# Kernel optimization log

Measured on AMD Instinct MI355X. Metric: run time of the kernel, lower is better.

## Reference

```python
import jax, jax.numpy as jnp
import numpy as np
import math

B, S, D, H, L = 4, 2048, 512, 8, 2
HD = D // H
NG = (3, 4, 5)
V = 30000          # n_gram_vocab_size
BASE = 31          # rolling hash base
NPATCH = 16
PLEN = S // NPATCH


def _ln(x, w, b, eps):
    m = x.mean(-1, keepdims=True)
    v = ((x - m) ** 2).mean(-1, keepdims=True)
    return (x - m) * jax.lax.rsqrt(v + eps) * w + b


def setup_inputs() -> dict:
    key = jax.random.key(0)
    ks = jax.random.split(key, 16)

    def nrm(i, shape, std=0.02):
        return jax.random.normal(ks[i], shape, dtype=jnp.float32) * std

    return {
        "byte_seq": jax.random.randint(ks[0], (B, S), 0, 256, dtype=jnp.int32),
        "patch_boundaries": jnp.arange(NPATCH + 1, dtype=jnp.int32) * PLEN,
        "byte_emb": nrm(1, (256, D), 1.0 / math.sqrt(D)),
        "ng_emb": nrm(2, (len(NG), V, D)),
        "tl_qkv_w": nrm(3, (L, 3 * D, D)),
        "tl_qkv_b": jnp.zeros((L, 3 * D), jnp.float32),
        "tl_out_w": nrm(4, (L, D, D)),
        "tl_out_b": jnp.zeros((L, D), jnp.float32),
        "tl_ln1_w": jnp.ones((L, D), jnp.float32),
        "tl_ln1_b": jnp.zeros((L, D), jnp.float32),
        "tl_ln2_w": jnp.ones((L, D), jnp.float32),
        "tl_ln2_b": jnp.zeros((L, D), jnp.float32),
        "tl_ff1_w": nrm(5, (L, 4 * D, D)),
        "tl_ff1_b": jnp.zeros((L, 4 * D), jnp.float32),
        "tl_ff2_w": nrm(6, (L, D, 4 * D)),
        "tl_ff2_b": jnp.zeros((L, D), jnp.float32),
        "ca_qkv_w": nrm(7, (3 * D, D)),
        "ca_qkv_b": jnp.zeros((3 * D,), jnp.float32),
        "ca_out_w": nrm(8, (D, D)),
        "ca_out_b": jnp.zeros((D,), jnp.float32),
        "ca_ln_w": jnp.ones((D,), jnp.float32),
        "ca_ln_b": jnp.zeros((D,), jnp.float32),
        "norm_w": jnp.ones((D,), jnp.float32),
        "norm_b": jnp.zeros((D,), jnp.float32),
    }


def _forward(byte_seq, patch_boundaries, byte_emb, ng_emb,
             tl_qkv_w, tl_qkv_b, tl_out_w, tl_out_b,
             tl_ln1_w, tl_ln1_b, tl_ln2_w, tl_ln2_b,
             tl_ff1_w, tl_ff1_b, tl_ff2_w, tl_ff2_b,
             ca_qkv_w, ca_qkv_b, ca_out_w, ca_out_b, ca_ln_w, ca_ln_b,
             norm_w, norm_b):
    x = byte_emb[byte_seq]                                  # [B,S,D]

    # n-gram rolling hash == polynomial hash mod V; computed in parallel
    # as windowed dot products with modular base powers (exact same values
    # as the sequential rolling-update loop in the torch code).
    ng_scale = 1.0 / (len(NG) + 1)
    for idx, n in enumerate(NG):
        powers = jnp.array([pow(BASE, n - 1 - i, V) for i in range(n)],
                           dtype=byte_seq.dtype)
        windows = jnp.stack([byte_seq[:, j:S - n + 1 + j] for j in range(n)],
                            axis=-1)                        # [B,S-n+1,n]
        h = (windows * powers).sum(-1) % V                   # [B,S-n+1]
        x = x.at[:, n - 1:].add(ng_emb[idx][h] * ng_scale)

    scale = 1.0 / math.sqrt(HD)
    neg = jnp.where(jnp.triu(jnp.ones((S, S), dtype=bool), 1),
                    -jnp.inf, 0.0).astype(x.dtype)           # causal additive mask

    # post-norm TransformerEncoderLayer (relu activation, dropout=0/eval)
    for l in range(L):
        qkv = x @ tl_qkv_w[l].T + tl_qkv_b[l]                # [B,S,3D]
        q, k, v = jnp.split(qkv, 3, axis=-1)
        q = q.reshape(B, S, H, HD).transpose(0, 2, 1, 3)
        k = k.reshape(B, S, H, HD).transpose(0, 2, 1, 3)
        v = v.reshape(B, S, H, HD).transpose(0, 2, 1, 3)
        scores = jnp.einsum('bhqd,bhkd->bhqk', q, k) * scale + neg
        a = jax.nn.softmax(scores, axis=-1)
        o = jnp.einsum('bhqk,bhkd->bhqd', a, v).transpose(0, 2, 1, 3).reshape(B, S, D)
        o = o @ tl_out_w[l].T + tl_out_b[l]
        x = _ln(x + o, tl_ln1_w[l], tl_ln1_b[l], 1e-5)
        ff = jax.nn.relu(x @ tl_ff1_w[l].T + tl_ff1_b[l]) @ tl_ff2_w[l].T + tl_ff2_b[l]
        x = _ln(x + ff, tl_ln2_w[l], tl_ln2_b[l], 1e-5)

    # uniform patch boundaries -> vectorized patch cross-attention
    npatch = patch_boundaries.shape[0] - 1
    plen = S // npatch
    xp = x.reshape(B, npatch, plen, D)
    query = xp.mean(axis=2)                                  # [B,P,D]
    qn = _ln(query, ca_ln_w, ca_ln_b, 1e-6)
    kvn = _ln(xp, ca_ln_w, ca_ln_b, 1e-6)
    wq, wk, wv = jnp.split(ca_qkv_w, 3, axis=0)
    bq, bk, bv = jnp.split(ca_qkv_b, 3)
    q = (qn @ wq.T + bq).reshape(B, npatch, H, HD)
    k = (kvn @ wk.T + bk).reshape(B, npatch, plen, H, HD)
    v = (kvn @ wv.T + bv).reshape(B, npatch, plen, H, HD)
    s = jnp.einsum('bphd,bplhd->bphl', q, k) * scale
    a = jax.nn.softmax(s, axis=-1)
    o = jnp.einsum('bphl,bplhd->bphd', a, v).reshape(B, npatch, D)
    patches = query + (o @ ca_out_w.T + ca_out_b)

    return _ln(x, norm_w, norm_b, 1e-6), _ln(patches, norm_w, norm_b, 1e-6)


def reference(byte_seq, patch_boundaries, byte_emb, ng_emb,
              tl_qkv_w, tl_qkv_b, tl_out_w, tl_out_b,
              tl_ln1_w, tl_ln1_b, tl_ln2_w, tl_ln2_b,
              tl_ff1_w, tl_ff1_b, tl_ff2_w, tl_ff2_b,
              ca_qkv_w, ca_qkv_b, ca_out_w, ca_out_b, ca_ln_w, ca_ln_b,
              norm_w, norm_b):
    return _forward(byte_seq, patch_boundaries, byte_emb, ng_emb,
                    tl_qkv_w, tl_qkv_b, tl_out_w, tl_out_b,
                    tl_ln1_w, tl_ln1_b, tl_ln2_w, tl_ln2_b,
                    tl_ff1_w, tl_ff1_b, tl_ff2_w, tl_ff2_b,
                    ca_qkv_w, ca_qkv_b, ca_out_w, ca_out_b, ca_ln_w, ca_ln_b,
                    norm_w, norm_b)
```

## Files before the change

kernel.cpp:

```cpp
#include <hip/hip_runtime.h>
#include <hip/hip_bf16.h>

#define B_ 4
#define S_ 2048
#define D_ 512
#define H_ 8
#define HD_ 64
#define L_ 2
#define V_ 30000
#define NPATCH_ 16
#define PLEN_ 128

typedef short bf16x8 __attribute__((ext_vector_type(8)));
typedef float f32x4 __attribute__((ext_vector_type(4)));

__device__ __forceinline__ unsigned short f2bf(float f) {
    unsigned u = __float_as_uint(f);
    return (unsigned short)((u + 0x7FFFu + ((u >> 16) & 1u)) >> 16);
}

__global__ __launch_bounds__(256) void cast_kernel(
    const float* __restrict__ src, unsigned short* __restrict__ dst, int n4)
{
    const int i = blockIdx.x * 256 + threadIdx.x;
    if (i >= n4) return;
    const float4 v = *reinterpret_cast<const float4*>(src + (size_t)i * 4);
    ushort4 o;
    o.x = f2bf(v.x); o.y = f2bf(v.y); o.z = f2bf(v.z); o.w = f2bf(v.w);
    *reinterpret_cast<ushort4*>(dst + (size_t)i * 4) = o;
}

__global__ __launch_bounds__(128) void embed_ngram_kernel(
    const int* __restrict__ bytes, const float* __restrict__ byte_emb,
    const float* __restrict__ ng_emb, float* __restrict__ x,
    unsigned short* __restrict__ xb)
{
    const int bs = blockIdx.x;
    const int s  = bs % S_;
    const int b  = bs / S_;
    const int d  = threadIdx.x * 4;
    const int* brow = bytes + (size_t)b * S_;

    const int c = brow[s];
    float4 v = *reinterpret_cast<const float4*>(byte_emb + (size_t)c * D_ + d);

    if (s >= 2) {
        int h = (brow[s-2]*961 + brow[s-1]*31 + brow[s]) % V_;
        const float4 g = *reinterpret_cast<const float4*>(ng_emb + ((size_t)0*V_ + h)*D_ + d);
        v.x += 0.25f*g.x; v.y += 0.25f*g.y; v.z += 0.25f*g.z; v.w += 0.25f*g.w;
    }
    if (s >= 3) {
        int h = (brow[s-3]*29791 + brow[s-2]*961 + brow[s-1]*31 + brow[s]) % V_;
        const float4 g = *reinterpret_cast<const float4*>(ng_emb + ((size_t)1*V_ + h)*D_ + d);
        v.x += 0.25f*g.x; v.y += 0.25f*g.y; v.z += 0.25f*g.z; v.w += 0.25f*g.w;
    }
    if (s >= 4) {
        int h = (brow[s-4]*23521 + brow[s-3]*29791 + brow[s-2]*961 + brow[s-1]*31 + brow[s]) % V_;
        const float4 g = *reinterpret_cast<const float4*>(ng_emb + ((size_t)2*V_ + h)*D_ + d);
        v.x += 0.25f*g.x; v.y += 0.25f*g.y; v.z += 0.25f*g.z; v.w += 0.25f*g.w;
    }
    *reinterpret_cast<float4*>(x + (size_t)bs * D_ + d) = v;
    ushort4 o;
    o.x = f2bf(v.x); o.y = f2bf(v.y); o.z = f2bf(v.z); o.w = f2bf(v.w);
    *reinterpret_cast<ushort4*>(xb + (size_t)bs * D_ + d) = o;
}

template<int DO_RELU, int BF16OUT>
__global__ __launch_bounds__(256) void mgemm_kernel(
    const unsigned short* __restrict__ Xb, const unsigned short* __restrict__ Wb,
    const float* __restrict__ bias, void* __restrict__ Yout,
    int M, int N, int K)
{
    __shared__ unsigned short As[128*64];
    __shared__ unsigned short Bs[128*64];

    const int t    = threadIdx.x;
    const int lane = t & 63;
    const int w    = t >> 6;
    const int bm   = blockIdx.y * 128, bn = blockIdx.x * 128;
    const int l15  = lane & 15, lg = lane >> 4;
    const int wr   = w >> 1, wc = w & 1;

    int srow[4], scol[4];
#pragma unroll
    for (int i = 0; i < 4; ++i) {
        const int off = w*1024 + i*4096 + lane*16;
        srow[i] = off >> 7;
        scol[i] = ((off >> 4) & 7) ^ (srow[i] & 7);
    }

    f32x4 acc[4][4];
#pragma unroll
    for (int mt = 0; mt < 4; ++mt)
#pragma unroll
        for (int nt = 0; nt < 4; ++nt) acc[mt][nt] = (f32x4){0.f,0.f,0.f,0.f};

    for (int kt = 0; kt < K; kt += 64) {
#pragma unroll
        for (int i = 0; i < 4; ++i) {
            const unsigned short* gA = Xb + (size_t)(bm + srow[i]) * K + kt + scol[i]*8;
            const unsigned short* gB = Wb + (size_t)(bn + srow[i]) * K + kt + scol[i]*8;
            __builtin_amdgcn_global_load_lds(
                (const __attribute__((address_space(1))) void*)gA,
                (__attribute__((address_space(3))) void*)&As[w*512 + i*2048], 16, 0, 0);
            __builtin_amdgcn_global_load_lds(
                (const __attribute__((address_space(1))) void*)gB,
                (__attribute__((address_space(3))) void*)&Bs[w*512 + i*2048], 16, 0, 0);
        }
        __syncthreads();

#pragma unroll
        for (int ks = 0; ks < 2; ++ks) {
            const int c16 = (ks*4 + lg) ^ (l15 & 7);
            bf16x8 a[4], b[4];
#pragma unroll
            for (int mt = 0; mt < 4; ++mt)
                a[mt] = *reinterpret_cast<const bf16x8*>(&As[(wr*64 + mt*16 + l15)*64 + c16*8]);
#pragma unroll
            for (int nt = 0; nt < 4; ++nt)
                b[nt] = *reinterpret_cast<const bf16x8*>(&Bs[(wc*64 + nt*16 + l15)*64 + c16*8]);
#pragma unroll
            for (int mt = 0; mt < 4; ++mt)
#pragma unroll
                for (int nt = 0; nt < 4; ++nt)
                    acc[mt][nt] = __builtin_amdgcn_mfma_f32_16x16x32_bf16(
                        a[mt], b[nt], acc[mt][nt], 0, 0, 0);
        }
        __syncthreads();
    }

    float bv[4];
#pragma unroll
    for (int nt = 0; nt < 4; ++nt) bv[nt] = bias[bn + wc*64 + nt*16 + l15];

#pragma unroll
    for (int mt = 0; mt < 4; ++mt) {
#pragma unroll
        for (int nt = 0; nt < 4; ++nt) {
            const int n = bn + wc*64 + nt*16 + l15;
#pragma unroll
            for (int r = 0; r < 4; ++r) {
                const int m = bm + wr*64 + mt*16 + 4*lg + r;
                float v = acc[mt][nt][r] + bv[nt];
                if (DO_RELU) v = fmaxf(v, 0.f);
                if (BF16OUT)
                    ((unsigned short*)Yout)[(size_t)m * N + n] = f2bf(v);
                else
                    ((float*)Yout)[(size_t)m * N + n] = v;
            }
        }
    }
}

__global__ __launch_bounds__(256) void gemm_kernel(
    const float* __restrict__ X, const float* __restrict__ W,
    const float* __restrict__ bias, const float* __restrict__ resid,
    float* __restrict__ Y, int M, int N, int K, int do_relu)
{
    __shared__ float As[16][68];
    __shared__ float Bs[16][68];
    const int tid = threadIdx.x;
    const int bm = blockIdx.y * 64, bn = blockIdx.x * 64;
    const int ty = tid >> 4, tx = tid & 15;
    const int lrow = tid >> 2, lc4 = (tid & 3) * 4;

    float acc[4][4];
#pragma unroll
    for (int i = 0; i < 4; ++i)
#pragma unroll
        for (int j = 0; j < 4; ++j) acc[i][j] = 0.f;

    for (int k0 = 0; k0 < K; k0 += 16) {
        const float4 xv = *reinterpret_cast<const float4*>(X + (size_t)(bm + lrow) * K + k0 + lc4);
        const float4 wv = *reinterpret_cast<const float4*>(W + (size_t)(bn + lrow) * K + k0 + lc4);
        __syncthreads();
        As[lc4+0][lrow] = xv.x; As[lc4+1][lrow] = xv.y;
        As[lc4+2][lrow] = xv.z; As[lc4+3][lrow] = xv.w;
        Bs[lc4+0][lrow] = wv.x; Bs[lc4+1][lrow] = wv.y;
        Bs[lc4+2][lrow] = wv.z; Bs[lc4+3][lrow] = wv.w;
        __syncthreads();
#pragma unroll
        for (int kk = 0; kk < 16; ++kk) {
            float a0 = As[kk][ty*4+0], a1 = As[kk][ty*4+1], a2 = As[kk][ty*4+2], a3 = As[kk][ty*4+3];
            float b0 = Bs[kk][tx*4+0], b1 = Bs[kk][tx*4+1], b2 = Bs[kk][tx*4+2], b3 = Bs[kk][tx*4+3];
            acc[0][0] += a0*b0; acc[0][1] += a0*b1; acc[0][2] += a0*b2; acc[0][3] += a0*b3;
            acc[1][0] += a1*b0; acc[1][1] += a1*b1; acc[1][2] += a1*b2; acc[1][3] += a1*b3;
            acc[2][0] += a2*b0; acc[2][1] += a2*b1; acc[2][2] += a2*b2; acc[2][3] += a2*b3;
            acc[3][0] += a3*b0; acc[3][1] += a3*b1; acc[3][2] += a3*b2; acc[3][3] += a3*b3;
        }
    }

#pragma unroll
    for (int i = 0; i < 4; ++i) {
        const int m = bm + ty*4 + i;
#pragma unroll
        for (int j = 0; j < 4; ++j) {
            const int n = bn + tx*4 + j;
            float v = acc[i][j] + bias[n];
            if (do_relu) v = fmaxf(v, 0.f);
            if (resid) v += resid[(size_t)m * N + n];
            Y[(size_t)m * N + n] = v;
        }
    }
}

__global__ __launch_bounds__(256) void attn_mfma_kernel(
    const unsigned short* __restrict__ qkvb, unsigned short* __restrict__ ob)
{
    __shared__ unsigned short Ks[64*72];
    __shared__ unsigned short Vt[64*72];
    __shared__ unsigned short Plds[4*16*72];

    const int t    = threadIdx.x;
    const int lane = t & 63;
    const int w    = t >> 6;
    const int qp   = blockIdx.x;
    const int bh   = blockIdx.y;
    const int h    = bh & 7;
    const int b    = bh >> 3;

    const unsigned short* base = qkvb + (size_t)b * S_ * 1536;
    const int l15 = lane & 15, lg = lane >> 4;
    const int skey = t >> 2, sd0 = (t & 3) * 16;
    const int sg = sd0 >> 4;
    const int scs = ((skey >> 3) ^ sg) * 8 + (skey & 7);
    unsigned short* pw_base = Plds + w*16*72;

#pragma unroll
    for (int half = 0; half < 2; ++half) {
        const int qb  = half ? (31 - qp) : qp;
        const int q0w = qb * 64 + w * 16;

        bf16x8 qf0, qf1;
        {
            const unsigned short* qr = base + (size_t)(q0w + l15) * 1536 + h*64 + lg*8;
            qf0 = *reinterpret_cast<const bf16x8*>(qr);
            qf1 = *reinterpret_cast<const bf16x8*>(qr + 32);
        }

        f32x4 oacc[4];
#pragma unroll
        for (int i = 0; i < 4; ++i) oacc[i] = (f32x4){0.f,0.f,0.f,0.f};
        float mrow[4] = {-INFINITY,-INFINITY,-INFINITY,-INFINITY};
        float lrow[4] = {0.f,0.f,0.f,0.f};

        const int ntiles = qb + 1;
        for (int tile = 0; tile < ntiles; ++tile) {
            const int kt = tile * 64;
            __syncthreads();
            {
                const unsigned short* srcK = base + (size_t)(kt + skey) * 1536 + 512  + h*64 + sd0;
                const unsigned short* srcV = base + (size_t)(kt + skey) * 1536 + 1024 + h*64 + sd0;
                *reinterpret_cast<bf16x8*>(&Ks[skey*72 + sd0])     = *reinterpret_cast<const bf16x8*>(srcK);
                *reinterpret_cast<bf16x8*>(&Ks[skey*72 + sd0 + 8]) = *reinterpret_cast<const bf16x8*>(srcK + 8);
                bf16x8 v0 = *reinterpret_cast<const bf16x8*>(srcV);
                bf16x8 v1 = *reinterpret_cast<const bf16x8*>(srcV + 8);
#pragma unroll
                for (int j = 0; j < 8; ++j) Vt[(sd0+j)*72 + scs]   = (unsigned short)v0[j];
#pragma unroll
                for (int j = 0; j < 8; ++j) Vt[(sd0+8+j)*72 + scs] = (unsigned short)v1[j];
            }
            __syncthreads();

            f32x4 sacc[4];
#pragma unroll
            for (int kt16 = 0; kt16 < 4; ++kt16) {
                sacc[kt16] = (f32x4){0.f,0.f,0.f,0.f};
                const unsigned short* kp = &Ks[(kt16*16 + l15)*72 + lg*8];
                bf16x8 k0 = *reinterpret_cast<const bf16x8*>(kp);
                bf16x8 k1 = *reinterpret_cast<const bf16x8*>(kp + 32);
                sacc[kt16] = __builtin_amdgcn_mfma_f32_16x16x32_bf16(qf0, k0, sacc[kt16], 0, 0, 0);
                sacc[kt16] = __builtin_amdgcn_mfma_f32_16x16x32_bf16(qf1, k1, sacc[kt16], 0, 0, 0);
            }

            const bool diag = (tile == ntiles - 1);
            float sv[4][4];
#pragma unroll
            for (int kt16 = 0; kt16 < 4; ++kt16) {
#pragma unroll
                for (int r = 0; r < 4; ++r) {
                    float s = sacc[kt16][r] * 0.125f;
                    if (diag) {
                        const int key = kt + kt16*16 + l15;
                        const int q   = q0w + 4*lg + r;
                        if (key > q) s = -INFINITY;
                    }
                    sv[kt16][r] = s;
                }
            }
#pragma unroll
            for (int r = 0; r < 4; ++r) {
                float tm = fmaxf(fmaxf(sv[0][r], sv[1][r]), fmaxf(sv[2][r], sv[3][r]));
#pragma unroll
                for (int off = 8; off; off >>= 1) tm = fmaxf(tm, __shfl_xor(tm, off, 64));
                const float nm = fmaxf(mrow[r], tm);
                const float al = __expf(mrow[r] - nm);
                mrow[r] = nm;
                float ps = 0.f;
#pragma unroll
                for (int kt16 = 0; kt16 < 4; ++kt16) {
                    const float p = __expf(sv[kt16][r] - nm);
                    ps += p;
                    pw_base[(4*lg + r)*72 + kt16*16 + l15] = f2bf(p);
                }
#pragma unroll
                for (int off = 8; off; off >>= 1) ps += __shfl_xor(ps, off, 64);
                lrow[r] = lrow[r]*al + ps;
#pragma unroll
                for (int dt = 0; dt < 4; ++dt) oacc[dt][r] *= al;
            }

            const unsigned short* pr = &pw_base[l15*72 + lg*8];
            bf16x8 pa0 = *reinterpret_cast<const bf16x8*>(pr);
            bf16x8 pa1 = *reinterpret_cast<const bf16x8*>(pr + 32);
#pragma unroll
            for (int dt = 0; dt < 4; ++dt) {
                const unsigned short* vp = &Vt[(dt*16 + l15)*72 + (lg ^ dt)*8];
                bf16x8 v0 = *reinterpret_cast<const bf16x8*>(vp);
                bf16x8 v1 = *reinterpret_cast<const bf16x8*>(vp + 32);
                oacc[dt] = __builtin_amdgcn_mfma_f32_16x16x32_bf16(pa0, v0, oacc[dt], 0, 0, 0);
                oacc[dt] = __builtin_amdgcn_mfma_f32_16x16x32_bf16(pa1, v1, oacc[dt], 0, 0, 0);
            }
        }

#pragma unroll
        for (int dt = 0; dt < 4; ++dt) {
#pragma unroll
            for (int r = 0; r < 4; ++r) {
                const int q = q0w + 4*lg + r;
                ob[((size_t)b*S_ + q)*D_ + h*64 + dt*16 + l15] = f2bf(oacc[dt][r] / lrow[r]);
            }
        }
    }
}

__global__ __launch_bounds__(256) void ln_kernel(
    float* __restrict__ dst, unsigned short* __restrict__ dst2,
    const float* __restrict__ src, const float* __restrict__ add,
    const float* __restrict__ w, const float* __restrict__ b, float eps)
{
    const int row = blockIdx.x, tid = threadIdx.x;
    const int lane = tid & 63, wave = tid >> 6;
    float2 v = *reinterpret_cast<const float2*>(src + (size_t)row * D_ + tid*2);
    if (add) {
        float2 a = *reinterpret_cast<const float2*>(add + (size_t)row * D_ + tid*2);
        v.x += a.x; v.y += a.y;
    }
    __shared__ float red[8];
    float s = v.x + v.y;
#pragma unroll
    for (int off = 32; off; off >>= 1) s += __shfl_xor(s, off, 64);
    if (lane == 0) red[wave] = s;
    __syncthreads();
    const float mean = (red[0]+red[1]+red[2]+red[3]) * (1.f/D_);
    const float d0 = v.x - mean, d1 = v.y - mean;
    float sq = d0*d0 + d1*d1;
#pragma unroll
    for (int off = 32; off; off >>= 1) sq += __shfl_xor(sq, off, 64);
    if (lane == 0) red[4+wave] = sq;
    __syncthreads();
    const float var = (red[4]+red[5]+red[6]+red[7]) * (1.f/D_);
    const float inv = rsqrtf(var + eps);
    const float o0 = d0*inv*w[tid*2] + b[tid*2];
    const float o1 = d1*inv*w[tid*2+1] + b[tid*2+1];
    *reinterpret_cast<float2*>(dst + (size_t)row * D_ + tid*2) = make_float2(o0, o1);
    if (dst2) {
        ushort2 u; u.x = f2bf(o0); u.y = f2bf(o1);
        *reinterpret_cast<ushort2*>(dst2 + (size_t)row * D_ + tid*2) = u;
    }
}

__global__ __launch_bounds__(256) void meanpool_kernel(
    const float* __restrict__ x, float* __restrict__ query)
{
    const int bp = blockIdx.x;
    const int d = threadIdx.x * 2;
    const float* base = x + (size_t)bp * PLEN_ * D_ + d;
    float s0 = 0.f, s1 = 0.f;
    for (int l = 0; l < PLEN_; ++l) {
        float2 v = *reinterpret_cast<const float2*>(base + (size_t)l * D_);
        s0 += v.x; s1 += v.y;
    }
    query[(size_t)bp*D_ + d]     = s0 * (1.f/PLEN_);
    query[(size_t)bp*D_ + d + 1] = s1 * (1.f/PLEN_);
}

__global__ __launch_bounds__(256) void patch_attn_kernel(
    const float* __restrict__ qbuf, const float* __restrict__ kv,
    float* __restrict__ o)
{
    const int wid  = blockIdx.x * 4 + (threadIdx.x >> 6);
    const int lane = threadIdx.x & 63;
    const int h  = wid % H_;
    const int bp = wid / H_;
    const float qv = qbuf[(size_t)bp*D_ + h*HD_ + lane] * 0.125f;
    const float* base = kv + (size_t)bp * PLEN_ * 1024 + h*HD_;

    float m = -INFINITY, l = 0.f, acc = 0.f;
    for (int t = 0; t < PLEN_; ++t) {
        const float* row = base + (size_t)t * 1024;
        float s = qv * row[lane];
#pragma unroll
        for (int off = 32; off; off >>= 1) s += __shfl_xor(s, off, 64);
        const float vv = row[512 + lane];
        const float nm = fmaxf(m, s);
        const float al = __expf(m - nm);
        const float p  = __expf(s - nm);
        l = l * al + p;
        acc = acc * al + p * vv;
        m = nm;
    }
    o[(size_t)bp*D_ + h*HD_ + lane] = acc / l;
}

extern "C" void kernel_launch(void* const* d_in, const int* in_sizes, int n_in,
                              void* d_out, int out_size, void* d_ws, size_t ws_size,
                              hipStream_t stream)
{
    const int*   byte_seq = (const int*)d_in[0];
    const float* byte_emb = (const float*)d_in[2];
    const float* ng_emb   = (const float*)d_in[3];
    const float* qkv_w = (const float*)d_in[4];
    const float* qkv_b = (const float*)d_in[5];
    const float* out_w = (const float*)d_in[6];
    const float* out_b = (const float*)d_in[7];
    const float* ln1_w = (const float*)d_in[8];
    const float* ln1_b = (const float*)d_in[9];
    const float* ln2_w = (const float*)d_in[10];
    const float* ln2_b = (const float*)d_in[11];
    const float* ff1_w = (const float*)d_in[12];
    const float* ff1_b = (const float*)d_in[13];
    const float* ff2_w = (const float*)d_in[14];
    const float* ff2_b = (const float*)d_in[15];
    const float* ca_qkv_w = (const float*)d_in[16];
    const float* ca_qkv_b = (const float*)d_in[17];
    const float* ca_out_w = (const float*)d_in[18];
    const float* ca_out_b = (const float*)d_in[19];
    const float* ca_ln_w  = (const float*)d_in[20];
    const float* ca_ln_b  = (const float*)d_in[21];
    const float* norm_w   = (const float*)d_in[22];
    const float* norm_b   = (const float*)d_in[23];
    float* out = (float*)d_out;

    char* ws = (char*)d_ws;
    const size_t MB = 1024*1024;
    float*          x     = (float*)(ws);
    char*           bufA  = ws + 16*MB;
    float*          bufB  = (float*)(ws + 48*MB);
    unsigned short* ob    = (unsigned short*)(ws + 64*MB);
    unsigned short* xb    = (unsigned short*)(ws + 72*MB);
    unsigned short* qkvw_b = (unsigned short*)(ws + 80*MB);
    unsigned short* outw_b = (unsigned short*)(ws + 83*MB);
    unsigned short* ff1w_b = (unsigned short*)(ws + 84*MB);
    unsigned short* ff2w_b = (unsigned short*)(ws + 88*MB);
    unsigned short* kvw_b  = (unsigned short*)(ws + 92*MB);
    float* query   = (float*)(ws + 93*MB);
    float* qn      = query + 64*512;
    float* qsm     = qn + 64*512;
    float* oca     = qsm + 64*512;
    float* patches = oca + 64*512;

    unsigned short* qkvb = (unsigned short*)bufA;
    unsigned short* ff1b = (unsigned short*)bufA;
    float*          kvf  = (float*)bufA;

    const int M = B_ * S_;

    cast_kernel<<<(2*1536*512/4)/256, 256, 0, stream>>>(qkv_w, qkvw_b, 2*1536*512/4);
    cast_kernel<<<(2*512*512/4)/256, 256, 0, stream>>>(out_w, outw_b, 2*512*512/4);
    cast_kernel<<<(2*2048*512/4)/256, 256, 0, stream>>>(ff1_w, ff1w_b, 2*2048*512/4);
    cast_kernel<<<(2*512*2048/4)/256, 256, 0, stream>>>(ff2_w, ff2w_b, 2*512*2048/4);
    cast_kernel<<<(1024*512/4)/256, 256, 0, stream>>>(ca_qkv_w + 512*512, kvw_b, 1024*512/4);

    embed_ngram_kernel<<<M, 128, 0, stream>>>(byte_seq, byte_emb, ng_emb, x, xb);

    for (int l = 0; l < L_; ++l) {
        mgemm_kernel<0,1><<<dim3(1536/128, M/128), 256, 0, stream>>>(
            xb, qkvw_b + (size_t)l*1536*D_, qkv_b + l*1536, qkvb, M, 1536, D_);
        attn_mfma_kernel<<<dim3(S_/128, B_*H_), 256, 0, stream>>>(qkvb, ob);
        mgemm_kernel<0,0><<<dim3(D_/128, M/128), 256, 0, stream>>>(
            ob, outw_b + (size_t)l*D_*D_, out_b + l*D_, bufB, M, D_, D_);
        ln_kernel<<<M, 256, 0, stream>>>(x, xb, x, bufB, ln1_w + l*D_, ln1_b + l*D_, 1e-5f);
        mgemm_kernel<1,1><<<dim3(2048/128, M/128), 256, 0, stream>>>(
            xb, ff1w_b + (size_t)l*2048*D_, ff1_b + l*2048, ff1b, M, 2048, D_);
        mgemm_kernel<0,0><<<dim3(D_/128, M/128), 256, 0, stream>>>(
            ff1b, ff2w_b + (size_t)l*D_*2048, ff2_b + l*D_, bufB, M, D_, 2048);
        ln_kernel<<<M, 256, 0, stream>>>(x, xb, x, bufB, ln2_w + l*D_, ln2_b + l*D_, 1e-5f);
    }

    meanpool_kernel<<<B_*NPATCH_, 256, 0, stream>>>(x, query);
    ln_kernel<<<B_*NPATCH_, 256, 0, stream>>>(qn, nullptr, query, nullptr, ca_ln_w, ca_ln_b, 1e-6f);
    ln_kernel<<<M, 256, 0, stream>>>(bufB, xb, x, nullptr, ca_ln_w, ca_ln_b, 1e-6f);
    mgemm_kernel<0,0><<<dim3(1024/128, M/128), 256, 0, stream>>>(
        xb, kvw_b, ca_qkv_b + 512, kvf, M, 1024, D_);
    gemm_kernel<<<dim3(D_/64, 1), 256, 0, stream>>>(
        qn, ca_qkv_w, ca_qkv_b, nullptr, qsm, 64, D_, D_, 0);
    patch_attn_kernel<<<B_*NPATCH_*H_/4, 256, 0, stream>>>(qsm, kvf, oca);
    gemm_kernel<<<dim3(D_/64, 1), 256, 0, stream>>>(
        oca, ca_out_w, ca_out_b, query, patches, 64, D_, D_, 0);

    ln_kernel<<<M, 256, 0, stream>>>(out, nullptr, x, nullptr, norm_w, norm_b, 1e-6f);
    ln_kernel<<<B_*NPATCH_, 256, 0, stream>>>(
        out + (size_t)M*D_, nullptr, patches, nullptr, norm_w, norm_b, 1e-6f);
}
```

Baseline: 620.8 us.

## Prefetch attention K/V tiles into registers, narrow N=512 GEMM tiles, fuse casts

Attention now loads the next K/V tile into registers while the current tile is computed, which overlaps global latency with MFMA work. The mgemm kernel takes a BN template parameter, and the N=512 GEMMs use 64-wide tiles so twice as many blocks fill the CUs. The five weight-cast launches are merged into one kernel. The costs are extra register pressure in attention and lower per-block reuse in the narrower GEMM tiles.

Result: faster. 570.6 us (-8.1%).

```diff
diff --git a/kernel.cpp b/kernel.cpp
--- a/kernel.cpp
+++ b/kernel.cpp
@@ -19,15 +19,31 @@
     return (unsigned short)((u + 0x7FFFu + ((u >> 16) & 1u)) >> 16);
 }
 
-__global__ __launch_bounds__(256) void cast_kernel(
-    const float* __restrict__ src, unsigned short* __restrict__ dst, int n4)
-{
-    const int i = blockIdx.x * 256 + threadIdx.x;
-    if (i >= n4) return;
-    const float4 v = *reinterpret_cast<const float4*>(src + (size_t)i * 4);
+#define C0_ (2*1536*512/4)
+#define C1_ (2*512*512/4)
+#define C2_ (2*2048*512/4)
+#define C3_ (2*512*2048/4)
+#define C4_ (1024*512/4)
+__global__ __launch_bounds__(256) void cast5_kernel(
+    const float* __restrict__ s0, const float* __restrict__ s1,
+    const float* __restrict__ s2, const float* __restrict__ s3,
+    const float* __restrict__ s4,
+    unsigned short* __restrict__ d0, unsigned short* __restrict__ d1,
+    unsigned short* __restrict__ d2, unsigned short* __restrict__ d3,
+    unsigned short* __restrict__ d4)
+{
+    int i = blockIdx.x * 256 + threadIdx.x;
+    const float* s; unsigned short* d;
+    if      (i < C0_)                  { s = s0; d = d0; }
+    else if ((i -= C0_) < C1_)         { s = s1; d = d1; }
+    else if ((i -= C1_) < C2_)         { s = s2; d = d2; }
+    else if ((i -= C2_) < C3_)         { s = s3; d = d3; }
+    else if ((i -= C3_) < C4_)         { s = s4; d = d4; }
+    else return;
+    const float4 v = *reinterpret_cast<const float4*>(s + (size_t)i * 4);
     ushort4 o;
     o.x = f2bf(v.x); o.y = f2bf(v.y); o.z = f2bf(v.z); o.w = f2bf(v.w);
-    *reinterpret_cast<ushort4*>(dst + (size_t)i * 4) = o;
+    *reinterpret_cast<ushort4*>(d + (size_t)i * 4) = o;
 }
 
 __global__ __launch_bounds__(128) void embed_ngram_kernel(
@@ -65,19 +81,21 @@
     *reinterpret_cast<ushort4*>(xb + (size_t)bs * D_ + d) = o;
 }
 
-template<int DO_RELU, int BF16OUT>
+template<int DO_RELU, int BF16OUT, int BN>
 __global__ __launch_bounds__(256) void mgemm_kernel(
     const unsigned short* __restrict__ Xb, const unsigned short* __restrict__ Wb,
     const float* __restrict__ bias, void* __restrict__ Yout,
     int M, int N, int K)
 {
+    constexpr int NT  = BN / 32;
+    constexpr int NLB = BN / 32;
     __shared__ unsigned short As[128*64];
-    __shared__ unsigned short Bs[128*64];
+    __shared__ unsigned short Bs[BN*64];
 
     const int t    = threadIdx.x;
     const int lane = t & 63;
     const int w    = t >> 6;
-    const int bm   = blockIdx.y * 128, bn = blockIdx.x * 128;
+    const int bm   = blockIdx.y * 128, bn = blockIdx.x * BN;
     const int l15  = lane & 15, lg = lane >> 4;
     const int wr   = w >> 1, wc = w & 1;
 
@@ -89,20 +107,23 @@
         scol[i] = ((off >> 4) & 7) ^ (srow[i] & 7);
     }
 
-    f32x4 acc[4][4];
+    f32x4 acc[4][NT];
 #pragma unroll
     for (int mt = 0; mt < 4; ++mt)
 #pragma unroll
-        for (int nt = 0; nt < 4; ++nt) acc[mt][nt] = (f32x4){0.f,0.f,0.f,0.f};
+        for (int nt = 0; nt < NT; ++nt) acc[mt][nt] = (f32x4){0.f,0.f,0.f,0.f};
 
     for (int kt = 0; kt < K; kt += 64) {
 #pragma unroll
         for (int i = 0; i < 4; ++i) {
             const unsigned short* gA = Xb + (size_t)(bm + srow[i]) * K + kt + scol[i]*8;
-            const unsigned short* gB = Wb + (size_t)(bn + srow[i]) * K + kt + scol[i]*8;
             __builtin_amdgcn_global_load_lds(
                 (const __attribute__((address_space(1))) void*)gA,
                 (__attribute__((address_space(3))) void*)&As[w*512 + i*2048], 16, 0, 0);
+        }
+#pragma unroll
+        for (int i = 0; i < NLB; ++i) {
+            const unsigned short* gB = Wb + (size_t)(bn + srow[i]) * K + kt + scol[i]*8;
             __builtin_amdgcn_global_load_lds(
                 (const __attribute__((address_space(1))) void*)gB,
                 (__attribute__((address_space(3))) void*)&Bs[w*512 + i*2048], 16, 0, 0);
@@ -112,32 +133,32 @@
 #pragma unroll
         for (int ks = 0; ks < 2; ++ks) {
             const int c16 = (ks*4 + lg) ^ (l15 & 7);
-            bf16x8 a[4], b[4];
+            bf16x8 a[4], b[NT];
 #pragma unroll
             for (int mt = 0; mt < 4; ++mt)
                 a[mt] = *reinterpret_cast<const bf16x8*>(&As[(wr*64 + mt*16 + l15)*64 + c16*8]);
 #pragma unroll
-            for (int nt = 0; nt < 4; ++nt)
-                b[nt] = *reinterpret_cast<const bf16x8*>(&Bs[(wc*64 + nt*16 + l15)*64 + c16*8]);
+            for (int nt = 0; nt < NT; ++nt)
+                b[nt] = *reinterpret_cast<const bf16x8*>(&Bs[(wc*(BN/2) + nt*16 + l15)*64 + c16*8]);
 #pragma unroll
             for (int mt = 0; mt < 4; ++mt)
 #pragma unroll
-                for (int nt = 0; nt < 4; ++nt)
+                for (int nt = 0; nt < NT; ++nt)
                     acc[mt][nt] = __builtin_amdgcn_mfma_f32_16x16x32_bf16(
                         a[mt], b[nt], acc[mt][nt], 0, 0, 0);
         }
         __syncthreads();
     }
 
-    float bv[4];
-#pragma unroll
-    for (int nt = 0; nt < 4; ++nt) bv[nt] = bias[bn + wc*64 + nt*16 + l15];
+    float bv[NT];
+#pragma unroll
+    for (int nt = 0; nt < NT; ++nt) bv[nt] = bias[bn + wc*(BN/2) + nt*16 + l15];
 
 #pragma unroll
     for (int mt = 0; mt < 4; ++mt) {
 #pragma unroll
-        for (int nt = 0; nt < 4; ++nt) {
-            const int n = bn + wc*64 + nt*16 + l15;
+        for (int nt = 0; nt < NT; ++nt) {
+            const int n = bn + wc*(BN/2) + nt*16 + l15;
 #pragma unroll
             for (int r = 0; r < 4; ++r) {
                 const int m = bm + wr*64 + mt*16 + 4*lg + r;
@@ -226,6 +247,16 @@
     const int scs = ((skey >> 3) ^ sg) * 8 + (skey & 7);
     unsigned short* pw_base = Plds + w*16*72;
 
+    bf16x8 k0r, k1r, v0r, v1r;
+#define LOADREG(KT) { \
+        const unsigned short* srcK_ = base + (size_t)((KT) + skey) * 1536 + 512 + h*64 + sd0; \
+        k0r = *reinterpret_cast<const bf16x8*>(srcK_); \
+        k1r = *reinterpret_cast<const bf16x8*>(srcK_ + 8); \
+        v0r = *reinterpret_cast<const bf16x8*>(srcK_ + 512); \
+        v1r = *reinterpret_cast<const bf16x8*>(srcK_ + 520); }
+
+    LOADREG(0);
+
 #pragma unroll
     for (int half = 0; half < 2; ++half) {
         const int qb  = half ? (31 - qp) : qp;
@@ -248,19 +279,15 @@
         for (int tile = 0; tile < ntiles; ++tile) {
             const int kt = tile * 64;
             __syncthreads();
-            {
-                const unsigned short* srcK = base + (size_t)(kt + skey) * 1536 + 512  + h*64 + sd0;
-                const unsigned short* srcV = base + (size_t)(kt + skey) * 1536 + 1024 + h*64 + sd0;
-                *reinterpret_cast<bf16x8*>(&Ks[skey*72 + sd0])     = *reinterpret_cast<const bf16x8*>(srcK);
-                *reinterpret_cast<bf16x8*>(&Ks[skey*72 + sd0 + 8]) = *reinterpret_cast<const bf16x8*>(srcK + 8);
-                bf16x8 v0 = *reinterpret_cast<const bf16x8*>(srcV);
-                bf16x8 v1 = *reinterpret_cast<const bf16x8*>(srcV + 8);
-#pragma unroll
-                for (int j = 0; j < 8; ++j) Vt[(sd0+j)*72 + scs]   = (unsigned short)v0[j];
-#pragma unroll
-                for (int j = 0; j < 8; ++j) Vt[(sd0+8+j)*72 + scs] = (unsigned short)v1[j];
-            }
+            *reinterpret_cast<bf16x8*>(&Ks[skey*72 + sd0])     = k0r;
+            *reinterpret_cast<bf16x8*>(&Ks[skey*72 + sd0 + 8]) = k1r;
+#pragma unroll
+            for (int j = 0; j < 8; ++j) Vt[(sd0+j)*72 + scs]   = (unsigned short)v0r[j];
+#pragma unroll
+            for (int j = 0; j < 8; ++j) Vt[(sd0+8+j)*72 + scs] = (unsigned short)v1r[j];
             __syncthreads();
+            const int nkt = (tile + 1 < ntiles) ? (kt + 64) : 0;
+            LOADREG(nkt);
 
             f32x4 sacc[4];
 #pragma unroll
@@ -332,6 +359,7 @@
             }
         }
     }
+#undef LOADREG
 }
 
 __global__ __launch_bounds__(256) void ln_kernel(
@@ -466,24 +494,22 @@
 
     const int M = B_ * S_;
 
-    cast_kernel<<<(2*1536*512/4)/256, 256, 0, stream>>>(qkv_w, qkvw_b, 2*1536*512/4);
-    cast_kernel<<<(2*512*512/4)/256, 256, 0, stream>>>(out_w, outw_b, 2*512*512/4);
-    cast_kernel<<<(2*2048*512/4)/256, 256, 0, stream>>>(ff1_w, ff1w_b, 2*2048*512/4);
-    cast_kernel<<<(2*512*2048/4)/256, 256, 0, stream>>>(ff2_w, ff2w_b, 2*512*2048/4);
-    cast_kernel<<<(1024*512/4)/256, 256, 0, stream>>>(ca_qkv_w + 512*512, kvw_b, 1024*512/4);
+    cast5_kernel<<<(C0_+C1_+C2_+C3_+C4_+255)/256, 256, 0, stream>>>(
+        qkv_w, out_w, ff1_w, ff2_w, ca_qkv_w + 512*512,
+        qkvw_b, outw_b, ff1w_b, ff2w_b, kvw_b);
 
     embed_ngram_kernel<<<M, 128, 0, stream>>>(byte_seq, byte_emb, ng_emb, x, xb);
 
     for (int l = 0; l < L_; ++l) {
-        mgemm_kernel<0,1><<<dim3(1536/128, M/128), 256, 0, stream>>>(
+        mgemm_kernel<0,1,128><<<dim3(1536/128, M/128), 256, 0, stream>>>(
             xb, qkvw_b + (size_t)l*1536*D_, qkv_b + l*1536, qkvb, M, 1536, D_);
         attn_mfma_kernel<<<dim3(S_/128, B_*H_), 256, 0, stream>>>(qkvb, ob);
-        mgemm_kernel<0,0><<<dim3(D_/128, M/128), 256, 0, stream>>>(
+        mgemm_kernel<0,0,64><<<dim3(D_/64, M/128), 256, 0, stream>>>(
             ob, outw_b + (size_t)l*D_*D_, out_b + l*D_, bufB, M, D_, D_);
         ln_kernel<<<M, 256, 0, stream>>>(x, xb, x, bufB, ln1_w + l*D_, ln1_b + l*D_, 1e-5f);
-        mgemm_kernel<1,1><<<dim3(2048/128, M/128), 256, 0, stream>>>(
+        mgemm_kernel<1,1,128><<<dim3(2048/128, M/128), 256, 0, stream>>>(
             xb, ff1w_b + (size_t)l*2048*D_, ff1_b + l*2048, ff1b, M, 2048, D_);
-        mgemm_kernel<0,0><<<dim3(D_/128, M/128), 256, 0, stream>>>(
+        mgemm_kernel<0,0,64><<<dim3(D_/64, M/128), 256, 0, stream>>>(
             ff1b, ff2w_b + (size_t)l*D_*2048, ff2_b + l*D_, bufB, M, D_, 2048);
         ln_kernel<<<M, 256, 0, stream>>>(x, xb, x, bufB, ln2_w + l*D_, ln2_b + l*D_, 1e-5f);
     }
@@ -491,7 +517,7 @@
     meanpool_kernel<<<B_*NPATCH_, 256, 0, stream>>>(x, query);
     ln_kernel<<<B_*NPATCH_, 256, 0, stream>>>(qn, nullptr, query, nullptr, ca_ln_w, ca_ln_b, 1e-6f);
     ln_kernel<<<M, 256, 0, stream>>>(bufB, xb, x, nullptr, ca_ln_w, ca_ln_b, 1e-6f);
-    mgemm_kernel<0,0><<<dim3(1024/128, M/128), 256, 0, stream>>>(
+    mgemm_kernel<0,0,128><<<dim3(1024/128, M/128), 256, 0, stream>>>(
         xb, kvw_b, ca_qkv_b + 512, kvf, M, 1024, D_);
     gemm_kernel<<<dim3(D_/64, 1), 256, 0, stream>>>(
         qn, ca_qkv_w, ca_qkv_b, nullptr, qsm, 64, D_, D_, 0);
```
